# Kernel tuning notes

Hardware: AMD Instinct MI355X
Metric: run time of the kernel (lower is better)

## Reference

```python
import jax, jax.numpy as jnp
import numpy as np

N_NODES = 100000
N_EDGES = 1600000
IN_CH = 256
OUT_CH = 128
EPS = 1e-12


def setup_inputs() -> dict:
    key = jax.random.key(0)
    k1, k2, k3 = jax.random.split(key, 3)
    x = jax.random.normal(k1, (N_NODES, IN_CH), dtype=jnp.float32)
    edge_index = jax.random.randint(k2, (2, N_EDGES), 0, N_NODES, dtype=jnp.int64)
    W = jax.random.normal(k3, (IN_CH, OUT_CH), dtype=jnp.float32) / np.float32(np.sqrt(IN_CH))
    b = jnp.zeros((OUT_CH,), dtype=jnp.float32)
    return {"x": x, "edge_index": edge_index, "W": W, "b": b}


def reference(x, edge_index, W, b):
    n = x.shape[0]
    # GCNConv: linear transform first, then normalized aggregation with self-loops
    h = x @ W  # [N, out]
    loops = jnp.arange(n, dtype=edge_index.dtype)
    row = jnp.concatenate([edge_index[0], loops])  # source nodes
    col = jnp.concatenate([edge_index[1], loops])  # destination nodes
    deg = jax.ops.segment_sum(jnp.ones_like(col, dtype=h.dtype), col, num_segments=n)
    dinv = jnp.where(deg > 0, jax.lax.rsqrt(jnp.maximum(deg, 1.0)), 0.0)  # deg^-1/2, inf->0
    wgt = dinv[row] * dinv[col]  # symmetric normalization per edge
    agg = jax.ops.segment_sum(h[row] * wgt[:, None], col, num_segments=n) + b  # [N, out]
    # min-max scale per node (dim=1)
    zmin = agg.min(axis=1, keepdims=True)
    zmax = agg.max(axis=1, keepdims=True)
    z = (agg - zmin) / (zmax - zmin)
    # F.normalize: L2 along dim=1 with eps clamp
    nrm = jnp.maximum(jnp.linalg.norm(z, axis=1, keepdims=True), EPS)
    return z / nrm
```

## Files before the change

kernel.cpp:

```cpp
#include <hip/hip_runtime.h>
#include <hip/hip_bf16.h>

#define N_NODES 100000
#define N_EDGES 1600000
#define IN_CH 256
#define OUT_CH 128

#define BSZ 256
#define NBUCK 391
#define BCAP 4736
#define CSC 4096
#define SCB 391
#define PREPB 64

#define GEMM_ROWS 64

typedef __attribute__((ext_vector_type(8))) short short8;
typedef __attribute__((ext_vector_type(4))) float floatx4;
typedef __attribute__((ext_vector_type(2))) float float2v;

union bfu { __hip_bfloat16 b; unsigned short u; };

__device__ inline unsigned short f2bf(float v) {
    bfu cv; cv.b = __float2bfloat16(v); return cv.u;
}
__device__ inline float bf2f(unsigned short u) {
    bfu cv; cv.u = u; return __bfloat162float(cv.b);
}

__device__ inline void pkacc(float2v& acc, unsigned g) {
    float2v v;
    v.x = __uint_as_float(g << 16);
    v.y = __uint_as_float(g & 0xffff0000u);
    asm("v_pk_add_f32 %0, %1, %2" : "=v"(acc) : "v"(v), "v"(acc));
}

__global__ __launch_bounds__(512) void k_scatter_prep(const int* __restrict__ rows,
                                                      const int* __restrict__ cols,
                                                      int* __restrict__ bcursor,
                                                      unsigned* __restrict__ ebuf,
                                                      const float* __restrict__ W,
                                                      unsigned short* __restrict__ wb_hi,
                                                      unsigned short* __restrict__ wb_lo) {
    if (blockIdx.x >= SCB) {
        int t = (blockIdx.x - SCB) * 512 + threadIdx.x;
        int j = t & 7;
        int lane = (t >> 3) & 63;
        int s = (t >> 9) & 7;
        int nt = t >> 12;
        int k = s * 32 + (lane >> 4) * 8 + j;
        int n = nt * 16 + (lane & 15);
        float w = W[k * OUT_CH + n];
        unsigned short hi = f2bf(w);
        wb_hi[t] = hi;
        wb_lo[t] = f2bf(w - bf2f(hi));
        return;
    }

    __shared__ int lcnt[NBUCK];
    __shared__ int lbase[NBUCK];
    int t = threadIdx.x;
    for (int i = t; i < NBUCK; i += 512) lcnt[i] = 0;
    __syncthreads();

    int s0 = blockIdx.x * CSC;
    int e1 = min(N_EDGES, s0 + CSC);

    unsigned val[8];
    int bkr[8], rk[8];
#pragma unroll
    for (int u = 0; u < 8; ++u) {
        int i = s0 + t + u * 512;
        bool p = i < e1;
        int c = p ? cols[i] : 0;
        int r = p ? rows[i] : 0;
        int bk = c >> 8;
        bkr[u] = bk;
        val[u] = ((unsigned)(c & (BSZ - 1)) << 17) | (unsigned)r;
        rk[u] = p ? atomicAdd(&lcnt[bk], 1) : 0;
    }
    __syncthreads();
    for (int i = t; i < NBUCK; i += 512) {
        int c = lcnt[i];
        lbase[i] = c ? atomicAdd(&bcursor[i], c) : 0;
    }
    __syncthreads();
#pragma unroll
    for (int u = 0; u < 8; ++u) {
        int i = s0 + t + u * 512;
        if (i < e1) ebuf[bkr[u] * BCAP + lbase[bkr[u]] + rk[u]] = val[u];
    }
}

__global__ __launch_bounds__(512) void pb_build(const unsigned* __restrict__ ebuf,
                                                const int* __restrict__ bcursor,
                                                int* __restrict__ cnt,
                                                int* __restrict__ base,
                                                float* __restrict__ dinv,
                                                int* __restrict__ es) {
    __shared__ int nh[BSZ];
    __shared__ int sc[BSZ];
    int t = threadIdx.x;
    int bk = blockIdx.x;
    int bb = bk * BCAP;
    int bc = bcursor[bk];
    if (t < BSZ) nh[t] = 0;
    __syncthreads();

    unsigned val[10];
    int rk[10];
#pragma unroll
    for (int u = 0; u < 10; ++u) {
        int i = t + u * 512;
        bool p = i < bc;
        unsigned v = p ? ebuf[bb + i] : 0u;
        val[u] = v;
        rk[u] = p ? atomicAdd(&nh[v >> 17], 1) : 0;
    }
    __syncthreads();
    if (t < BSZ) sc[t] = nh[t];
    __syncthreads();
    for (int off = 1; off < BSZ; off <<= 1) {
        int v = (t < BSZ && t >= off) ? sc[t - off] : 0;
        __syncthreads();
        if (t < BSZ) sc[t] += v;
        __syncthreads();
    }
    if (t < BSZ) {
        int node = bk * BSZ + t;
        if (node < N_NODES) {
            int c = nh[t];
            cnt[node] = c;
            base[node] = bb + sc[t] - c;
            dinv[node] = rsqrtf((float)(c + 1));
        }
    }
#pragma unroll
    for (int u = 0; u < 10; ++u) {
        int i = t + u * 512;
        if (i < bc) {
            unsigned v = val[u];
            int dl = v >> 17;
            es[bb + sc[dl] - nh[dl] + rk[u]] = (int)(v & 0x1FFFFu) << 8;
        }
    }
}

__global__ __launch_bounds__(512) void k_gemm(const float* __restrict__ x,
                                              const unsigned short* __restrict__ wb_hi,
                                              const unsigned short* __restrict__ wb_lo,
                                              const float* __restrict__ dinv,
                                              unsigned short* __restrict__ hbs) {
    __shared__ short8 xbh[4 * 8 * 68];
    __shared__ short8 xbl[4 * 8 * 68];
    int t = threadIdx.x;
    int wv = t >> 6;
    int lane = t & 63;
    int row0 = blockIdx.x * GEMM_ROWS;

    short8 Bh[8], Bl[8];
    const short8* bhp = (const short8*)wb_hi + (size_t)wv * 8 * 64 + lane;
    const short8* blp = (const short8*)wb_lo + (size_t)wv * 8 * 64 + lane;
#pragma unroll
    for (int s = 0; s < 8; ++s) {
        Bh[s] = bhp[s * 64];
        Bl[s] = blp[s * 64];
    }

#pragma unroll
    for (int q = 0; q < 4; ++q) {
        int c = q * 512 + t;
        int row = c >> 5;
        int cc  = c & 31;
        int gr = min(row0 + row, N_NODES - 1);
        const float4* xp = (const float4*)(x + (size_t)gr * IN_CH + cc * 8);
        float4 v0 = xp[0];
        float4 v1 = xp[1];
        float xv[8] = {v0.x, v0.y, v0.z, v0.w, v1.x, v1.y, v1.z, v1.w};
        short8 hh, ll;
#pragma unroll
        for (int j = 0; j < 8; ++j) {
            unsigned short hi = f2bf(xv[j]);
            hh[j] = (short)hi;
            ll[j] = (short)f2bf(xv[j] - bf2f(hi));
        }
        int ms = row >> 4, r15 = row & 15, s = cc >> 2, q2 = cc & 3;
        int idx = (ms * 8 + s) * 68 + q2 * 17 + r15;
        xbh[idx] = hh;
        xbl[idx] = ll;
    }
    __syncthreads();

    int r15 = lane & 15;
    int quad = lane >> 4;
    int lidx = quad * 17 + r15;

    floatx4 acc[4];
#pragma unroll
    for (int ms = 0; ms < 4; ++ms) {
        acc[ms] = (floatx4){0.f, 0.f, 0.f, 0.f};
#pragma unroll
        for (int s = 0; s < 8; ++s) {
            short8 ah = xbh[(ms * 8 + s) * 68 + lidx];
            short8 al = xbl[(ms * 8 + s) * 68 + lidx];
            acc[ms] = __builtin_amdgcn_mfma_f32_16x16x32_bf16(ah, Bh[s], acc[ms], 0, 0, 0);
            acc[ms] = __builtin_amdgcn_mfma_f32_16x16x32_bf16(ah, Bl[s], acc[ms], 0, 0, 0);
            acc[ms] = __builtin_amdgcn_mfma_f32_16x16x32_bf16(al, Bh[s], acc[ms], 0, 0, 0);
        }
    }

#pragma unroll
    for (int ms = 0; ms < 4; ++ms)
#pragma unroll
        for (int r = 0; r < 4; ++r) {
            int row = row0 + ms * 16 + quad * 4 + r;
            if (row < N_NODES) {
                size_t idx = (size_t)row * OUT_CH + wv * 16 + r15;
                hbs[idx] = f2bf(acc[ms][r] * dinv[row]);
            }
        }
}

__global__ __launch_bounds__(256) void k_agg_fin(const unsigned short* __restrict__ hbs,
                                                 const float* __restrict__ dinv,
                                                 const int* __restrict__ es,
                                                 const int* __restrict__ base,
                                                 const int* __restrict__ cnt,
                                                 const float* __restrict__ b,
                                                 float* __restrict__ out) {
    int t = threadIdx.x;
    int lane = t & 63;
    int ll = lane & 15;
    int node = blockIdx.x * 16 + (t >> 4);

    const char* hb = (const char*)hbs;
    int lane_byte = ll << 4;
    int bidx = (lane & 48) << 2;

    float dn = dinv[node];
    int d  = cnt[node];
    int st = base[node];

    float4 bv0 = ((const float4*)b)[ll * 2];
    float4 bv1 = ((const float4*)b)[ll * 2 + 1];

    uint4 gs = *(const uint4*)(hb + ((size_t)node << 8) + lane_byte);
    float2v acc[4];
    acc[0].x = __uint_as_float(gs.x << 16); acc[0].y = __uint_as_float(gs.x & 0xffff0000u);
    acc[1].x = __uint_as_float(gs.y << 16); acc[1].y = __uint_as_float(gs.y & 0xffff0000u);
    acc[2].x = __uint_as_float(gs.z << 16); acc[2].y = __uint_as_float(gs.z & 0xffff0000u);
    acc[3].x = __uint_as_float(gs.w << 16); acc[3].y = __uint_as_float(gs.w & 0xffff0000u);

    int dm = d;
    dm = max(dm, __shfl_xor(dm, 16, 64));
    dm = max(dm, __shfl_xor(dm, 32, 64));
    int iters = __builtin_amdgcn_readfirstlane((dm + 15) >> 4);

    const int zoff = N_NODES << 8;

    for (int it = 0; it < iters; ++it) {
        int jb = it << 4;
        int off = zoff;
        if (jb + ll < d) off = es[st + jb + ll];

        uint4 ga[4], gb[4];
#pragma unroll
        for (int k = 0; k < 4; ++k) {
            int ro = __builtin_amdgcn_ds_bpermute(bidx + (k << 2), off);
            ga[k] = *(const uint4*)(hb + (unsigned)(ro + lane_byte));
        }
#pragma unroll
        for (int k = 0; k < 4; ++k) {
            int ro = __builtin_amdgcn_ds_bpermute(bidx + ((4 + k) << 2), off);
            gb[k] = *(const uint4*)(hb + (unsigned)(ro + lane_byte));
        }
#pragma unroll
        for (int k = 0; k < 4; ++k) {
            pkacc(acc[0], ga[k].x); pkacc(acc[1], ga[k].y);
            pkacc(acc[2], ga[k].z); pkacc(acc[3], ga[k].w);
        }
#pragma unroll
        for (int k = 0; k < 4; ++k) {
            int ro = __builtin_amdgcn_ds_bpermute(bidx + ((8 + k) << 2), off);
            ga[k] = *(const uint4*)(hb + (unsigned)(ro + lane_byte));
        }
#pragma unroll
        for (int k = 0; k < 4; ++k) {
            pkacc(acc[0], gb[k].x); pkacc(acc[1], gb[k].y);
            pkacc(acc[2], gb[k].z); pkacc(acc[3], gb[k].w);
        }
#pragma unroll
        for (int k = 0; k < 4; ++k) {
            int ro = __builtin_amdgcn_ds_bpermute(bidx + ((12 + k) << 2), off);
            gb[k] = *(const uint4*)(hb + (unsigned)(ro + lane_byte));
        }
#pragma unroll
        for (int k = 0; k < 4; ++k) {
            pkacc(acc[0], ga[k].x); pkacc(acc[1], ga[k].y);
            pkacc(acc[2], ga[k].z); pkacc(acc[3], ga[k].w);
        }
#pragma unroll
        for (int k = 0; k < 4; ++k) {
            pkacc(acc[0], gb[k].x); pkacc(acc[1], gb[k].y);
            pkacc(acc[2], gb[k].z); pkacc(acc[3], gb[k].w);
        }
    }

    float v[8];
    v[0] = dn * acc[0].x + bv0.x;  v[1] = dn * acc[0].y + bv0.y;
    v[2] = dn * acc[1].x + bv0.z;  v[3] = dn * acc[1].y + bv0.w;
    v[4] = dn * acc[2].x + bv1.x;  v[5] = dn * acc[2].y + bv1.y;
    v[6] = dn * acc[3].x + bv1.z;  v[7] = dn * acc[3].y + bv1.w;

    float lmin = v[0], lmax = v[0];
#pragma unroll
    for (int i = 1; i < 8; ++i) { lmin = fminf(lmin, v[i]); lmax = fmaxf(lmax, v[i]); }
#pragma unroll
    for (int m = 8; m; m >>= 1) {
        lmin = fminf(lmin, __shfl_xor(lmin, m, 64));
        lmax = fmaxf(lmax, __shfl_xor(lmax, m, 64));
    }
    float scale = 1.0f / (lmax - lmin);
    float z[8];
    float ss = 0.f;
#pragma unroll
    for (int i = 0; i < 8; ++i) { z[i] = (v[i] - lmin) * scale; ss += z[i] * z[i]; }
#pragma unroll
    for (int m = 8; m; m >>= 1) ss += __shfl_xor(ss, m, 64);
    float inv = 1.0f / fmaxf(sqrtf(ss), 1e-12f);

    float4 o0 = {z[0] * inv, z[1] * inv, z[2] * inv, z[3] * inv};
    float4 o1 = {z[4] * inv, z[5] * inv, z[6] * inv, z[7] * inv};
    float4* op = (float4*)(out + (size_t)node * OUT_CH);
    op[ll * 2] = o0;
    op[ll * 2 + 1] = o1;
}

extern "C" void kernel_launch(void* const* d_in, const int* in_sizes, int n_in,
                              void* d_out, int out_size, void* d_ws, size_t ws_size,
                              hipStream_t stream) {
    const float* x = (const float*)d_in[0];
    const int* ei = (const int*)d_in[1];
    const float* W = (const float*)d_in[2];
    const float* b = (const float*)d_in[3];
    float* out = (float*)d_out;

    char* ws = (char*)d_ws;
    size_t o = 0;
    auto alloc = [&](size_t bytes) { void* p = ws + o; o = (o + bytes + 255) & ~(size_t)255; return p; };
    float* dinv    = (float*)alloc((size_t)N_NODES * 4);
    int*   cnt     = (int*)  alloc((size_t)N_NODES * 4);
    int*   base    = (int*)  alloc((size_t)N_NODES * 4);
    int*   bcursor = (int*)  alloc(NBUCK * 4);
    unsigned short* wb_hi = (unsigned short*)alloc((size_t)IN_CH * OUT_CH * 2);
    unsigned short* wb_lo = (unsigned short*)alloc((size_t)IN_CH * OUT_CH * 2);
    unsigned short* hbs = (unsigned short*)alloc((size_t)(N_NODES + 1) * OUT_CH * 2);
    unsigned* ebuf = (unsigned*)alloc((size_t)NBUCK * BCAP * 4);
    int*   es      = (int*)  alloc((size_t)NBUCK * BCAP * 4);

    const int* rows = ei;
    const int* cols = ei + N_EDGES;

    hipMemsetAsync(bcursor, 0, NBUCK * sizeof(int), stream);
    hipMemsetAsync(hbs + (size_t)N_NODES * OUT_CH, 0, OUT_CH * 2, stream);

    k_scatter_prep<<<SCB + PREPB, 512, 0, stream>>>(rows, cols, bcursor, ebuf,
                                                    W, wb_hi, wb_lo);

    pb_build<<<NBUCK, 512, 0, stream>>>(ebuf, bcursor, cnt, base, dinv, es);

    k_gemm<<<(N_NODES + GEMM_ROWS - 1) / GEMM_ROWS, 512, 0, stream>>>(
        x, wb_hi, wb_lo, dinv, hbs);

    k_agg_fin<<<N_NODES / 16, 256, 0, stream>>>(hbs, dinv, es, base, cnt, b, out);
}
```

Baseline: 290.4 us.

## Fuse edge scatter with GEMM and move source dinv scaling into aggregation

The dinv[row] scaling is taken out of the GEMM and applied instead inside the aggregation, via a prefetched per-edge dinv gather broadcast with ds_bpermute and packed FMA. With that dependency gone, the GEMM can run in the same kernel as the edge bucket scatter, before pb_build, and the two memsets become a small init kernel. The GEMM tile shrinks to 32 rows. This removes kernel launches and a serialization point, and lets the GEMM overlap the scatter. The cost is an extra dinv gather and bpermute per edge in the aggregation loop.

```diff
diff --git a/kernel.cpp b/kernel.cpp
--- a/kernel.cpp
+++ b/kernel.cpp
@@ -13,7 +13,8 @@
 #define SCB 391
 #define PREPB 64
 
-#define GEMM_ROWS 64
+#define GEMM_ROWS 32
+#define GEMB 3125
 
 typedef __attribute__((ext_vector_type(8))) short short8;
 typedef __attribute__((ext_vector_type(4))) float floatx4;
@@ -28,68 +29,146 @@
     bfu cv; cv.u = u; return __bfloat162float(cv.b);
 }
 
-__device__ inline void pkacc(float2v& acc, unsigned g) {
+__device__ inline void pkfma(float2v& acc, unsigned g, float2v dnp) {
     float2v v;
     v.x = __uint_as_float(g << 16);
     v.y = __uint_as_float(g & 0xffff0000u);
-    asm("v_pk_add_f32 %0, %1, %2" : "=v"(acc) : "v"(v), "v"(acc));
-}
-
-__global__ __launch_bounds__(512) void k_scatter_prep(const int* __restrict__ rows,
-                                                      const int* __restrict__ cols,
-                                                      int* __restrict__ bcursor,
-                                                      unsigned* __restrict__ ebuf,
-                                                      const float* __restrict__ W,
-                                                      unsigned short* __restrict__ wb_hi,
-                                                      unsigned short* __restrict__ wb_lo) {
-    if (blockIdx.x >= SCB) {
-        int t = (blockIdx.x - SCB) * 512 + threadIdx.x;
-        int j = t & 7;
-        int lane = (t >> 3) & 63;
-        int s = (t >> 9) & 7;
-        int nt = t >> 12;
-        int k = s * 32 + (lane >> 4) * 8 + j;
-        int n = nt * 16 + (lane & 15);
-        float w = W[k * OUT_CH + n];
-        unsigned short hi = f2bf(w);
-        wb_hi[t] = hi;
-        wb_lo[t] = f2bf(w - bf2f(hi));
-        return;
-    }
-
+    asm("v_pk_fma_f32 %0, %1, %2, %3" : "=v"(acc) : "v"(v), "v"(dnp), "v"(acc));
+}
+
+__global__ __launch_bounds__(512) void k_init(const float* __restrict__ W,
+                                              unsigned short* __restrict__ wb_hi,
+                                              unsigned short* __restrict__ wb_lo,
+                                              int* __restrict__ bcursor,
+                                              unsigned* __restrict__ zrow) {
+    int tid = threadIdx.x;
+    if (blockIdx.x == 0 && tid < NBUCK) bcursor[tid] = 0;
+    if (blockIdx.x == 1 && tid < 64) zrow[tid] = 0;
+
+    int t = blockIdx.x * 512 + tid;
+    int j = t & 7;
+    int lane = (t >> 3) & 63;
+    int s = (t >> 9) & 7;
+    int nt = t >> 12;
+    int k = s * 32 + (lane >> 4) * 8 + j;
+    int n = nt * 16 + (lane & 15);
+    float w = W[k * OUT_CH + n];
+    unsigned short hi = f2bf(w);
+    wb_hi[t] = hi;
+    wb_lo[t] = f2bf(w - bf2f(hi));
+}
+
+__global__ __launch_bounds__(512) void k_main(const int* __restrict__ rows,
+                                              const int* __restrict__ cols,
+                                              int* __restrict__ bcursor,
+                                              unsigned* __restrict__ ebuf,
+                                              const float* __restrict__ x,
+                                              const unsigned short* __restrict__ wb_hi,
+                                              const unsigned short* __restrict__ wb_lo,
+                                              unsigned short* __restrict__ hbs) {
     __shared__ int lcnt[NBUCK];
     __shared__ int lbase[NBUCK];
+    __shared__ short8 xbh[2 * 8 * 68];
+    __shared__ short8 xbl[2 * 8 * 68];
+
     int t = threadIdx.x;
-    for (int i = t; i < NBUCK; i += 512) lcnt[i] = 0;
+
+    if (blockIdx.x < SCB) {
+        if (t < NBUCK) lcnt[t] = 0;
+        __syncthreads();
+
+        int s0 = blockIdx.x * CSC;
+        int e1 = min(N_EDGES, s0 + CSC);
+
+        unsigned val[8];
+        int bkr[8], rk[8];
+#pragma unroll
+        for (int u = 0; u < 8; ++u) {
+            int i = s0 + t + u * 512;
+            bool p = i < e1;
+            int c = p ? cols[i] : 0;
+            int r = p ? rows[i] : 0;
+            int bk = c >> 8;
+            bkr[u] = bk;
+            val[u] = ((unsigned)(c & (BSZ - 1)) << 17) | (unsigned)r;
+            rk[u] = p ? atomicAdd(&lcnt[bk], 1) : 0;
+        }
+        __syncthreads();
+        if (t < NBUCK) {
+            int c = lcnt[t];
+            lbase[t] = c ? atomicAdd(&bcursor[t], c) : 0;
+        }
+        __syncthreads();
+#pragma unroll
+        for (int u = 0; u < 8; ++u) {
+            int i = s0 + t + u * 512;
+            if (i < e1) ebuf[bkr[u] * BCAP + lbase[bkr[u]] + rk[u]] = val[u];
+        }
+        return;
+    }
+
+    int wv = t >> 6;
+    int lane = t & 63;
+    int row0 = (blockIdx.x - SCB) * GEMM_ROWS;
+
+    short8 Bh[8], Bl[8];
+    const short8* bhp = (const short8*)wb_hi + (size_t)wv * 8 * 64 + lane;
+    const short8* blp = (const short8*)wb_lo + (size_t)wv * 8 * 64 + lane;
+#pragma unroll
+    for (int s = 0; s < 8; ++s) {
+        Bh[s] = bhp[s * 64];
+        Bl[s] = blp[s * 64];
+    }
+
+#pragma unroll
+    for (int q = 0; q < 2; ++q) {
+        int c = q * 512 + t;
+        int row = c >> 5;
+        int cc  = c & 31;
+        const float4* xp = (const float4*)(x + (size_t)(row0 + row) * IN_CH + cc * 8);
+        float4 v0 = xp[0];
+        float4 v1 = xp[1];
+        float xv[8] = {v0.x, v0.y, v0.z, v0.w, v1.x, v1.y, v1.z, v1.w};
+        short8 hh, ll;
+#pragma unroll
+        for (int j = 0; j < 8; ++j) {
+            unsigned short hi = f2bf(xv[j]);
+            hh[j] = (short)hi;
+            ll[j] = (short)f2bf(xv[j] - bf2f(hi));
+        }
+        int ms = row >> 4, r15 = row & 15, s = cc >> 2, q2 = cc & 3;
+        int idx = (ms * 8 + s) * 68 + q2 * 17 + r15;
+        xbh[idx] = hh;
+        xbl[idx] = ll;
+    }
     __syncthreads();
 
-    int s0 = blockIdx.x * CSC;
-    int e1 = min(N_EDGES, s0 + CSC);
-
-    unsigned val[8];
-    int bkr[8], rk[8];
-#pragma unroll
-    for (int u = 0; u < 8; ++u) {
-        int i = s0 + t + u * 512;
-        bool p = i < e1;
-        int c = p ? cols[i] : 0;
-        int r = p ? rows[i] : 0;
-        int bk = c >> 8;
-        bkr[u] = bk;
-        val[u] = ((unsigned)(c & (BSZ - 1)) << 17) | (unsigned)r;
-        rk[u] = p ? atomicAdd(&lcnt[bk], 1) : 0;
-    }
-    __syncthreads();
-    for (int i = t; i < NBUCK; i += 512) {
-        int c = lcnt[i];
-        lbase[i] = c ? atomicAdd(&bcursor[i], c) : 0;
-    }
-    __syncthreads();
-#pragma unroll
-    for (int u = 0; u < 8; ++u) {
-        int i = s0 + t + u * 512;
-        if (i < e1) ebuf[bkr[u] * BCAP + lbase[bkr[u]] + rk[u]] = val[u];
-    }
+    int r15 = lane & 15;
+    int quad = lane >> 4;
+    int lidx = quad * 17 + r15;
+
+    floatx4 acc[2];
+#pragma unroll
+    for (int ms = 0; ms < 2; ++ms) {
+        acc[ms] = (floatx4){0.f, 0.f, 0.f, 0.f};
+#pragma unroll
+        for (int s = 0; s < 8; ++s) {
+            short8 ah = xbh[(ms * 8 + s) * 68 + lidx];
+            short8 al = xbl[(ms * 8 + s) * 68 + lidx];
+            acc[ms] = __builtin_amdgcn_mfma_f32_16x16x32_bf16(ah, Bh[s], acc[ms], 0, 0, 0);
+            acc[ms] = __builtin_amdgcn_mfma_f32_16x16x32_bf16(ah, Bl[s], acc[ms], 0, 0, 0);
+            acc[ms] = __builtin_amdgcn_mfma_f32_16x16x32_bf16(al, Bh[s], acc[ms], 0, 0, 0);
+        }
+    }
+
+#pragma unroll
+    for (int ms = 0; ms < 2; ++ms)
+#pragma unroll
+        for (int r = 0; r < 4; ++r) {
+            int row = row0 + ms * 16 + quad * 4 + r;
+            size_t idx = (size_t)row * OUT_CH + wv * 16 + r15;
+            hbs[idx] = f2bf(acc[ms][r]);
+        }
 }
 
 __global__ __launch_bounds__(512) void pb_build(const unsigned* __restrict__ ebuf,
@@ -146,81 +225,6 @@
     }
 }
 
-__global__ __launch_bounds__(512) void k_gemm(const float* __restrict__ x,
-                                              const unsigned short* __restrict__ wb_hi,
-                                              const unsigned short* __restrict__ wb_lo,
-                                              const float* __restrict__ dinv,
-                                              unsigned short* __restrict__ hbs) {
-    __shared__ short8 xbh[4 * 8 * 68];
-    __shared__ short8 xbl[4 * 8 * 68];
-    int t = threadIdx.x;
-    int wv = t >> 6;
-    int lane = t & 63;
-    int row0 = blockIdx.x * GEMM_ROWS;
-
-    short8 Bh[8], Bl[8];
-    const short8* bhp = (const short8*)wb_hi + (size_t)wv * 8 * 64 + lane;
-    const short8* blp = (const short8*)wb_lo + (size_t)wv * 8 * 64 + lane;
-#pragma unroll
-    for (int s = 0; s < 8; ++s) {
-        Bh[s] = bhp[s * 64];
-        Bl[s] = blp[s * 64];
-    }
-
-#pragma unroll
-    for (int q = 0; q < 4; ++q) {
-        int c = q * 512 + t;
-        int row = c >> 5;
-        int cc  = c & 31;
-        int gr = min(row0 + row, N_NODES - 1);
-        const float4* xp = (const float4*)(x + (size_t)gr * IN_CH + cc * 8);
-        float4 v0 = xp[0];
-        float4 v1 = xp[1];
-        float xv[8] = {v0.x, v0.y, v0.z, v0.w, v1.x, v1.y, v1.z, v1.w};
-        short8 hh, ll;
-#pragma unroll
-        for (int j = 0; j < 8; ++j) {
-            unsigned short hi = f2bf(xv[j]);
-            hh[j] = (short)hi;
-            ll[j] = (short)f2bf(xv[j] - bf2f(hi));
-        }
-        int ms = row >> 4, r15 = row & 15, s = cc >> 2, q2 = cc & 3;
-        int idx = (ms * 8 + s) * 68 + q2 * 17 + r15;
-        xbh[idx] = hh;
-        xbl[idx] = ll;
-    }
-    __syncthreads();
-
-    int r15 = lane & 15;
-    int quad = lane >> 4;
-    int lidx = quad * 17 + r15;
-
-    floatx4 acc[4];
-#pragma unroll
-    for (int ms = 0; ms < 4; ++ms) {
-        acc[ms] = (floatx4){0.f, 0.f, 0.f, 0.f};
-#pragma unroll
-        for (int s = 0; s < 8; ++s) {
-            short8 ah = xbh[(ms * 8 + s) * 68 + lidx];
-            short8 al = xbl[(ms * 8 + s) * 68 + lidx];
-            acc[ms] = __builtin_amdgcn_mfma_f32_16x16x32_bf16(ah, Bh[s], acc[ms], 0, 0, 0);
-            acc[ms] = __builtin_amdgcn_mfma_f32_16x16x32_bf16(ah, Bl[s], acc[ms], 0, 0, 0);
-            acc[ms] = __builtin_amdgcn_mfma_f32_16x16x32_bf16(al, Bh[s], acc[ms], 0, 0, 0);
-        }
-    }
-
-#pragma unroll
-    for (int ms = 0; ms < 4; ++ms)
-#pragma unroll
-        for (int r = 0; r < 4; ++r) {
-            int row = row0 + ms * 16 + quad * 4 + r;
-            if (row < N_NODES) {
-                size_t idx = (size_t)row * OUT_CH + wv * 16 + r15;
-                hbs[idx] = f2bf(acc[ms][r] * dinv[row]);
-            }
-        }
-}
-
 __global__ __launch_bounds__(256) void k_agg_fin(const unsigned short* __restrict__ hbs,
                                                  const float* __restrict__ dinv,
                                                  const int* __restrict__ es,
@@ -234,6 +238,7 @@
     int node = blockIdx.x * 16 + (t >> 4);
 
     const char* hb = (const char*)hbs;
+    const char* dvc = (const char*)dinv;
     int lane_byte = ll << 4;
     int bidx = (lane & 48) << 2;
 
@@ -245,11 +250,12 @@
     float4 bv1 = ((const float4*)b)[ll * 2 + 1];
 
     uint4 gs = *(const uint4*)(hb + ((size_t)node << 8) + lane_byte);
+    float2v dself; dself.x = dn; dself.y = dn;
     float2v acc[4];
-    acc[0].x = __uint_as_float(gs.x << 16); acc[0].y = __uint_as_float(gs.x & 0xffff0000u);
-    acc[1].x = __uint_as_float(gs.y << 16); acc[1].y = __uint_as_float(gs.y & 0xffff0000u);
-    acc[2].x = __uint_as_float(gs.z << 16); acc[2].y = __uint_as_float(gs.z & 0xffff0000u);
-    acc[3].x = __uint_as_float(gs.w << 16); acc[3].y = __uint_as_float(gs.w & 0xffff0000u);
+#pragma unroll
+    for (int c = 0; c < 4; ++c) { acc[c].x = 0.f; acc[c].y = 0.f; }
+    pkfma(acc[0], gs.x, dself); pkfma(acc[1], gs.y, dself);
+    pkfma(acc[2], gs.z, dself); pkfma(acc[3], gs.w, dself);
 
     int dm = d;
     dm = max(dm, __shfl_xor(dm, 16, 64));
@@ -258,52 +264,73 @@
 
     const int zoff = N_NODES << 8;
 
+    int off = zoff; float dnv = 0.f;
+    if (ll < d) {
+        off = es[st + ll];
+        dnv = *(const float*)(dvc + ((unsigned)off >> 6));
+    }
+
     for (int it = 0; it < iters; ++it) {
-        int jb = it << 4;
-        int off = zoff;
-        if (jb + ll < d) off = es[st + jb + ll];
+        int offn = zoff; float dnn = 0.f;
+        int jb2 = (it + 1) << 4;
+        if (jb2 + ll < d) {
+            offn = es[st + jb2 + ll];
+            dnn = *(const float*)(dvc + ((unsigned)offn >> 6));
+        }
+        int dni = __float_as_int(dnv);
 
         uint4 ga[4], gb[4];
+        float2v da[4], db[4];
 #pragma unroll
         for (int k = 0; k < 4; ++k) {
             int ro = __builtin_amdgcn_ds_bpermute(bidx + (k << 2), off);
+            float f = __int_as_float(__builtin_amdgcn_ds_bpermute(bidx + (k << 2), dni));
+            da[k].x = f; da[k].y = f;
             ga[k] = *(const uint4*)(hb + (unsigned)(ro + lane_byte));
         }
 #pragma unroll
         for (int k = 0; k < 4; ++k) {
             int ro = __builtin_amdgcn_ds_bpermute(bidx + ((4 + k) << 2), off);
+            float f = __int_as_float(__builtin_amdgcn_ds_bpermute(bidx + ((4 + k) << 2), dni));
+            db[k].x = f; db[k].y = f;
             gb[k] = *(const uint4*)(hb + (unsigned)(ro + lane_byte));
         }
 #pragma unroll
         for (int k = 0; k < 4; ++k) {
-            pkacc(acc[0], ga[k].x); pkacc(acc[1], ga[k].y);
-            pkacc(acc[2], ga[k].z); pkacc(acc[3], ga[k].w);
+            pkfma(acc[0], ga[k].x, da[k]); pkfma(acc[1], ga[k].y, da[k]);
+            pkfma(acc[2], ga[k].z, da[k]); pkfma(acc[3], ga[k].w, da[k]);
         }
 #pragma unroll
         for (int k = 0; k < 4; ++k) {
             int ro = __builtin_amdgcn_ds_bpermute(bidx + ((8 + k) << 2), off);
+            float f = __int_as_float(__builtin_amdgcn_ds_bpermute(bidx + ((8 + k) << 2), dni));
+            da[k].x = f; da[k].y = f;
             ga[k] = *(const uint4*)(hb + (unsigned)(ro + lane_byte));
         }
 #pragma unroll
         for (int k = 0; k < 4; ++k) {
-            pkacc(acc[0], gb[k].x); pkacc(acc[1], gb[k].y);
-            pkacc(acc[2], gb[k].z); pkacc(acc[3], gb[k].w);
+            pkfma(acc[0], gb[k].x, db[k]); pkfma(acc[1], gb[k].y, db[k]);
+            pkfma(acc[2], gb[k].z, db[k]); pkfma(acc[3], gb[k].w, db[k]);
         }
 #pragma unroll
         for (int k = 0; k < 4; ++k) {
             int ro = __builtin_amdgcn_ds_bpermute(bidx + ((12 + k) << 2), off);
+            float f = __int_as_float(__builtin_amdgcn_ds_bpermute(bidx + ((12 + k) << 2), dni));
+            db[k].x = f; db[k].y = f;
             gb[k] = *(const uint4*)(hb + (unsigned)(ro + lane_byte));
         }
 #pragma unroll
         for (int k = 0; k < 4; ++k) {
-            pkacc(acc[0], ga[k].x); pkacc(acc[1], ga[k].y);
-            pkacc(acc[2], ga[k].z); pkacc(acc[3], ga[k].w);
-        }
-#pragma unroll
-        for (int k = 0; k < 4; ++k) {
-            pkacc(acc[0], gb[k].x); pkacc(acc[1], gb[k].y);
-            pkacc(acc[2], gb[k].z); pkacc(acc[3], gb[k].w);
-        }
+            pkfma(acc[0], ga[k].x, da[k]); pkfma(acc[1], ga[k].y, da[k]);
+            pkfma(acc[2], ga[k].z, da[k]); pkfma(acc[3], ga[k].w, da[k]);
+        }
+#pragma unroll
+        for (int k = 0; k < 4; ++k) {
+            pkfma(acc[0], gb[k].x, db[k]); pkfma(acc[1], gb[k].y, db[k]);
+            pkfma(acc[2], gb[k].z, db[k]); pkfma(acc[3], gb[k].w, db[k]);
+        }
+
+        off = offn; dnv = dnn;
     }
 
     float v[8];
@@ -361,16 +388,13 @@
     const int* rows = ei;
     const int* cols = ei + N_EDGES;
 
-    hipMemsetAsync(bcursor, 0, NBUCK * sizeof(int), stream);
-    hipMemsetAsync(hbs + (size_t)N_NODES * OUT_CH, 0, OUT_CH * 2, stream);
-
-    k_scatter_prep<<<SCB + PREPB, 512, 0, stream>>>(rows, cols, bcursor, ebuf,
-                                                    W, wb_hi, wb_lo);
+    k_init<<<PREPB, 512, 0, stream>>>(W, wb_hi, wb_lo, bcursor,
+                                      (unsigned*)(hbs + (size_t)N_NODES * OUT_CH));
+
+    k_main<<<SCB + GEMB, 512, 0, stream>>>(rows, cols, bcursor, ebuf,
+                                           x, wb_hi, wb_lo, hbs);
 
     pb_build<<<NBUCK, 512, 0, stream>>>(ebuf, bcursor, cnt, base, dinv, es);
 
-    k_gemm<<<(N_NODES + GEMM_ROWS - 1) / GEMM_ROWS, 512, 0, stream>>>(
-        x, wb_hi, wb_lo, dinv, hbs);
-
     k_agg_fin<<<N_NODES / 16, 256, 0, stream>>>(hbs, dinv, es, base, cnt, b, out);
 }
```

Result: faster. 273.4 us (-5.8%).
